# Kernel tuning notes

Measured on AMD Instinct MI355X. Metric: run time of the kernel, lower is better.

The kernel has to match this reference:

```python
import jax, jax.numpy as jnp
import numpy as np
from jax import lax

B = 8192
HS = 64        # hidden_size (output channels)
HS4 = HS + 4   # internal channel count (68)
K = 3          # conv kernel size


def setup_inputs() -> dict:
    key = jax.random.key(0)
    ks = jax.random.split(key, 16)
    def n(k, shape, s=1.0):
        return jax.random.normal(k, shape, dtype=jnp.float32) * s
    return {
        "x": n(ks[0], (B, HS, 6, 6)),
        "cell": n(ks[1], (B, 2)),
        "interspace_coord": n(ks[2], (B, 2, 6, 6)),
        "conv1_w": n(ks[3], (HS4, HS4, K, K), 0.05),
        "conv1_b": n(ks[4], (HS4,), 0.05),
        "conv3_w": n(ks[5], (HS4, HS4, K, K), 0.05),
        "conv3_b": n(ks[6], (HS4,), 0.05),
        "lin5_w": n(ks[7], (9 * HS, HS4 * 25), 0.02),
        "lin5_b": n(ks[8], (9 * HS,), 0.02),
        "lin4_w": n(ks[9], (9 * HS, HS4 * 16), 0.02),
        "lin4_b": n(ks[10], (9 * HS,), 0.02),
        "lin3_w": n(ks[11], (9 * HS, HS4 * 9), 0.02),
        "lin3_b": n(ks[12], (9 * HS,), 0.02),
        "final_w": n(ks[13], (HS, 9 * HS), 0.02),
        "final_b": n(ks[14], (HS,), 0.02),
    }


def _conv(z, w, b):
    # torch Conv2d with padding=k//2, stride 1 == SAME conv, NCHW/OIHW
    y = lax.conv_general_dilated(z, w, (1, 1), 'SAME',
                                 dimension_numbers=('NCHW', 'OIHW', 'NCHW'))
    return y + b[None, :, None, None]


def _corners(z, ws):
    # four corner windows, stacked on a new leading axis (corner-major)
    H, W = z.shape[-2:]
    return jnp.stack([z[..., :ws, :ws],
                      z[..., :ws, W - ws:],
                      z[..., H - ws:, :ws],
                      z[..., H - ws:, W - ws:]], axis=0)


def reference(x, cell, interspace_coord,
              conv1_w, conv1_b, conv3_w, conv3_b,
              lin5_w, lin5_b, lin4_w, lin4_b, lin3_w, lin3_b,
              final_w, final_b):
    Bn = x.shape[0]
    new_cell = jnp.broadcast_to(cell.reshape(Bn, -1)[:, :, None, None],
                                (Bn, 2, 6, 6))
    lins = {5: (lin5_w, lin5_b), 4: (lin4_w, lin4_b), 3: (lin3_w, lin3_b)}
    for ws in (5, 4, 3):
        z = jnp.concatenate([x, new_cell, interspace_coord], axis=1)  # [B,68,6,6]
        z = _corners(z, ws).reshape(-1, HS4, ws, ws)                  # [4B,68,ws,ws]
        z = jnp.sin(z) + jnp.cos(z)
        z = jax.nn.relu(_conv(z, conv1_w, conv1_b))
        z = jnp.sin(z) + jnp.cos(z)
        z = jax.nn.relu(_conv(z, conv3_w, conv3_b)).reshape(4, Bn, -1)
        Wl, bl = lins[ws]
        z = jax.nn.relu(z @ Wl.T + bl).reshape(4, Bn, HS, 3, 3)
        m = jnp.concatenate([z[0], z[1]], axis=-1)   # [B,64,3,6]
        n = jnp.concatenate([z[2], z[3]], axis=-1)
        x = jnp.concatenate([m, n], axis=-2)          # [B,64,6,6]
    ew = 3
    c = _corners(x, ew)                               # [4,B,64,3,3]
    c = c.reshape(4 * Bn, -1) @ final_w.T + final_b   # [4B,64]
    c = c.reshape(Bn, HS, 2, 2)                       # same flat-order reshape as torch
    xc = x[:, :, ew - 1:ew + 1, ew - 1:ew + 1]        # center 2x2
    return (xc * c).reshape(Bn, HS, -1)
```

## Files before the change

kernel.cpp:

```cpp
#include <hip/hip_runtime.h>
#include <hip/hip_bf16.h>
#include <cstdint>
#include <cstddef>

#define BN 8192
#define MTOT 32768

using bf16 = __hip_bfloat16;
typedef float f32x4 __attribute__((ext_vector_type(4)));
typedef short short8 __attribute__((ext_vector_type(8)));

__device__ __forceinline__ bf16 f2b(float v) { return __float2bfloat16(v); }
__device__ __forceinline__ float b2f(bf16 v) { return __bfloat162float(v); }
__device__ __forceinline__ float sincos_sum(float x) {
    return 1.41421356237f * __sinf(x + 0.78539816340f);
}

template<int WS> struct WsCfg;
template<> struct WsCfg<5> { static constexpr int KD = 1728, NP = 1792, KTRUE = 1700; };
template<> struct WsCfg<4> { static constexpr int KD = 1088, NP = 1152, KTRUE = 1088; };
template<> struct WsCfg<3> { static constexpr int KD = 640,  NP = 640,  KTRUE = 612;  };

template<int WS, bool SRC_F32>
__global__ __launch_bounds__(256)
void zprep_block(const float* __restrict__ xF, const bf16* __restrict__ xB,
                 const float* __restrict__ cell, const float* __restrict__ isc,
                 bf16* __restrict__ Z, int m0g, int CM)
{
    constexpr int KD = WsCfg<WS>::KD;
    constexpr int KTRUE = 68 * WS * WS;
    const int b = blockIdx.x, tid = threadIdx.x;
    __shared__ float s[68][37];

    for (int i = tid; i < 64 * 36; i += 256) {
        int ic = i / 36, off = i % 36;
        size_t idx = ((size_t)b * 64 + ic) * 36 + off;
        float t = SRC_F32 ? xF[idx] : b2f(xB[idx]);
        s[ic][off] = sincos_sum(t);
    }
    if (tid < 2) {
        float t = sincos_sum(cell[b * 2 + tid]);
        #pragma unroll
        for (int off = 0; off < 36; off++) s[64 + tid][off] = t;
    }
    if (tid >= 64 && tid < 136) {
        int j = tid - 64;
        int ic = j / 36, off = j % 36;
        s[66 + ic][off] = sincos_sum(isc[((size_t)b * 2 + ic) * 36 + off]);
    }
    __syncthreads();

    for (int i = tid; i < 4 * KD; i += 256) {
        int q = i / KD, k = i % KD;
        int gm = q * BN + b;
        if (gm < m0g || gm >= m0g + CM) continue;
        float v = 0.f;
        if (k < KTRUE) {
            int pi = k / 68, ic = k % 68;
            int r = (q >> 1) * (6 - WS) + pi / WS;
            int c = (q & 1) * (6 - WS) + pi % WS;
            v = s[ic][r * 6 + c];
        }
        Z[(size_t)(gm - m0g) * KD + k] = f2b(v);
    }
}

template<int WS>
__global__ void build_wdense(const float* __restrict__ w1, const float* __restrict__ w3,
                             bf16* __restrict__ W1d, bf16* __restrict__ W3d)
{
    constexpr int KD = WsCfg<WS>::KD, NP = WsCfg<WS>::NP;
    constexpr int KTRUE = 68 * WS * WS;
    constexpr unsigned per = (unsigned)NP * (unsigned)KD;
    unsigned e = blockIdx.x * 256u + threadIdx.x;
    if (e >= 2u * per) return;
    const float* src = (e < per) ? w1 : w3;
    bf16* dst = (e < per) ? W1d : W3d;
    unsigned i = (e < per) ? e : (e - per);
    int n = (int)(i / (unsigned)KD), k = (int)(i % (unsigned)KD);
    float v = 0.f;
    if (n < KTRUE && k < KTRUE) {
        int po = n / 68, oc = n % 68, ro = po / WS, co = po % WS;
        int pi = k / 68, ic = k % 68, ri = pi / WS, ci = pi % WS;
        int kr = ri - ro + 1, kc = ci - co + 1;
        if (kr >= 0 && kr < 3 && kc >= 0 && kc < 3)
            v = src[((oc * 68 + ic) * 3 + kr) * 3 + kc];
    }
    dst[i] = f2b(v);
}

template<int WS>
__global__ void repack_lin(const float* __restrict__ wl, bf16* __restrict__ WlP)
{
    constexpr int KD = WsCfg<WS>::KD;
    constexpr int KTRUE = 68 * WS * WS;
    unsigned e = blockIdx.x * 256u + threadIdx.x;
    if (e >= 640u * (unsigned)KD) return;
    int n = (int)(e / (unsigned)KD), k = (int)(e % (unsigned)KD);
    float v = 0.f;
    if (n < 576 && k < KTRUE) {
        int pi = k / 68, ic = k % 68;
        v = wl[(size_t)n * KTRUE + ic * (WS * WS) + pi];
    }
    WlP[e] = f2b(v);
}

__global__ void repack_fin(const float* __restrict__ fw, bf16* __restrict__ WfP)
{
    unsigned e = blockIdx.x * 256u + threadIdx.x;
    if (e >= 128u * 576u) return;
    unsigned n = e / 576u, k = e % 576u;
    WfP[e] = (n < 64u) ? f2b(fw[n * 576u + k]) : f2b(0.f);
}

__global__ void build_bias(const float* __restrict__ b1, const float* __restrict__ b3,
                           const float* __restrict__ bl5, const float* __restrict__ bl4,
                           const float* __restrict__ bl3, const float* __restrict__ bfin,
                           float* __restrict__ bias)
{
    int e = blockIdx.x * 256 + threadIdx.x;
    if (e >= 9216) return;
    float v = 0.f;
    if (e < 1792)      { int n = e;        if (n < 1700) v = b1[n % 68]; }
    else if (e < 3584) { int n = e - 1792; if (n < 1700) v = b3[n % 68]; }
    else if (e < 4736) { int n = e - 3584; if (n < 1088) v = b1[n % 68]; }
    else if (e < 5888) { int n = e - 4736; if (n < 1088) v = b3[n % 68]; }
    else if (e < 6528) { int n = e - 5888; if (n < 612)  v = b1[n % 68]; }
    else if (e < 7168) { int n = e - 6528; if (n < 612)  v = b3[n % 68]; }
    else if (e < 7808) { int n = e - 7168; if (n < 576)  v = bl5[n]; }
    else if (e < 8448) { int n = e - 7808; if (n < 576)  v = bl4[n]; }
    else if (e < 9088) { int n = e - 8448; if (n < 576)  v = bl3[n]; }
    else               { int n = e - 9088; if (n < 64)   v = bfin[n]; }
    bias[e] = v;
}

__global__ void afin_prep(const bf16* __restrict__ xb, bf16* __restrict__ Afin,
                          int m_start, int CM)
{
    unsigned e = blockIdx.x * 256u + threadIdx.x;
    if (e >= (unsigned)CM * 576u) return;
    int lm = (int)(e / 576u), k = (int)(e % 576u);
    int m = m_start + lm;
    int q = m >> 13, b = m & (BN - 1);
    int ch = k / 9, p = k % 9, pr = p / 3, pc = p % 3;
    int r = (q >> 1) * 3 + pr, c = (q & 1) * 3 + pc;
    Afin[e] = xb[((size_t)b * 64 + ch) * 36 + r * 6 + c];
}

__device__ __forceinline__ void gload_lds16(const bf16* g, const bf16* lds_wave_base)
{
    unsigned off = (unsigned)(uintptr_t)lds_wave_base;
    off = __builtin_amdgcn_readfirstlane(off);
    __builtin_amdgcn_global_load_lds((const __attribute__((address_space(1))) unsigned int*)g,
                                     (__attribute__((address_space(3))) unsigned int*)off,
                                     16, 0, 0);
}

__device__ __forceinline__ int imin(int a, int b) { return a < b ? a : b; }
__device__ __forceinline__ int imax(int a, int b) { return a > b ? a : b; }

template<int EPI, int WS>
__global__ __launch_bounds__(256)
void gemm_bt(const bf16* __restrict__ A, const bf16* __restrict__ Bm, int KD,
             const float* __restrict__ bias, int ntiles,
             bf16* __restrict__ C, int ldc, int nlimit,
             int m0g, bf16* __restrict__ xbuf_out,
             const bf16* __restrict__ xbuf_xc, float* __restrict__ outp)
{
    __shared__ bf16 As[128 * 32];
    __shared__ bf16 Bs[128 * 32];
    const int tid = threadIdx.x;
    const int wave = tid >> 6, lane = tid & 63;
    const int l15 = lane & 15, lq = lane >> 4;
    const int wr = (wave >> 1) * 64, wc = (wave & 1) * 64;

    const int id = blockIdx.x;
    const int mt8 = (int)gridDim.x / (ntiles * 8);
    const int xcd = id & 7, local = id >> 3;
    const int m_idx = xcd * mt8 + local / ntiles;
    const int n_idx = local % ntiles;
    const int n0 = n_idx * 128, m0 = m_idx * 128;

    int klo = 0, khi = KD;
    if (WS > 0) {
        constexpr int ROWLEN = WS * 68;
        int po_lo = imin(n0 / 68, WS * WS - 1);
        int po_hi = imin((n0 + 127) / 68, WS * WS - 1);
        int r_lo = imax(po_lo / WS - 1, 0);
        int r_hi = imin(po_hi / WS + 1, WS - 1);
        klo = (r_lo * ROWLEN) & ~31;
        khi = imin(KD, ((r_hi + 1) * ROWLEN + 31) & ~31);
    }

    const bf16* Ab = A + (size_t)m0 * KD;
    const bf16* Bb = Bm + (size_t)n0 * KD;
    const int srow = tid >> 2, scol = (tid & 3) * 8;
    const bf16* aG0 = Ab + (size_t)srow * KD + scol;
    const bf16* aG1 = Ab + (size_t)(srow + 64) * KD + scol;
    const bf16* bG0 = Bb + (size_t)srow * KD + scol;
    const bf16* bG1 = Bb + (size_t)(srow + 64) * KD + scol;
    const bf16* lA0 = &As[wave * 512];
    const bf16* lA1 = &As[2048 + wave * 512];
    const bf16* lB0 = &Bs[wave * 512];
    const bf16* lB1 = &Bs[2048 + wave * 512];

    f32x4 acc[4][4];
    #pragma unroll
    for (int i = 0; i < 4; i++)
        #pragma unroll
        for (int j = 0; j < 4; j++) { f32x4 z = {0.f, 0.f, 0.f, 0.f}; acc[i][j] = z; }

    for (int k0 = klo; k0 < khi; k0 += 32) {
        gload_lds16(aG0 + k0, lA0);
        gload_lds16(aG1 + k0, lA1);
        gload_lds16(bG0 + k0, lB0);
        gload_lds16(bG1 + k0, lB1);
        __syncthreads();
        short8 af[4], bg[4];
        #pragma unroll
        for (int i = 0; i < 4; i++) af[i] = *(const short8*)&As[(wr + i * 16 + l15) * 32 + lq * 8];
        #pragma unroll
        for (int j = 0; j < 4; j++) bg[j] = *(const short8*)&Bs[(wc + j * 16 + l15) * 32 + lq * 8];
        #pragma unroll
        for (int i = 0; i < 4; i++)
            #pragma unroll
            for (int j = 0; j < 4; j++)
                acc[i][j] = __builtin_amdgcn_mfma_f32_16x16x32_bf16(af[i], bg[j], acc[i][j], 0, 0, 0);
        __syncthreads();
    }

    #pragma unroll
    for (int i = 0; i < 4; i++) {
        #pragma unroll
        for (int j = 0; j < 4; j++) {
            int n = n0 + wc + j * 16 + l15;
            #pragma unroll
            for (int r = 0; r < 4; r++) {
                int m = m0 + wr + i * 16 + lq * 4 + r;
                float v = acc[i][j][r];
                if (EPI == 0) {
                    if (n < nlimit) {
                        v += bias[n]; v = fmaxf(v, 0.f); v = sincos_sum(v);
                        C[(size_t)m * ldc + n] = f2b(v);
                    }
                } else if (EPI == 1) {
                    if (n < nlimit) {
                        v += bias[n]; v = fmaxf(v, 0.f);
                        C[(size_t)m * ldc + n] = f2b(v);
                    }
                } else if (EPI == 2) {
                    if (n < 576) {
                        v += bias[n]; v = fmaxf(v, 0.f);
                        int gm = m0g + m;
                        int q = gm >> 13, b = gm & (BN - 1);
                        int ch = n / 9, p = n % 9, rr = p / 3, cc = p % 3;
                        int R = rr + (q >> 1) * 3, Cc = cc + (q & 1) * 3;
                        xbuf_out[((size_t)b * 64 + ch) * 36 + R * 6 + Cc] = f2b(v);
                    }
                } else {
                    if (n < 64) {
                        v += bias[n];
                        int gm = m0g + m;
                        int f = gm * 64 + n;
                        int b2 = f >> 8, rem = f & 255;
                        int ch2 = rem >> 2, ii = (rem >> 1) & 1, jj = rem & 1;
                        float xc = b2f(xbuf_xc[((size_t)b2 * 64 + ch2) * 36 + (2 + ii) * 6 + (2 + jj)]);
                        outp[f] = v * xc;
                    }
                }
            }
        }
    }
}

template<int WS, bool SRC_F32>
static void run_ws(const float* xsrcF, const bf16* xsrcB, bf16* xdst,
                   const float* cell, const float* isc,
                   bf16* Za, bf16* Zb, const bf16* W1d, const bf16* W3d, const bf16* WlP,
                   const float* bias, int bo1, int bo3, int bol,
                   int nchunk, hipStream_t stream)
{
    constexpr int KD = WsCfg<WS>::KD, NP = WsCfg<WS>::NP;
    int CM = MTOT / nchunk;
    int mt = CM / 128;
    for (int c = 0; c < nchunk; c++) {
        int m0g = c * CM;
        zprep_block<WS, SRC_F32><<<BN, 256, 0, stream>>>(
            xsrcF, xsrcB, cell, isc, Za, m0g, CM);
        int nt12 = NP / 128;
        gemm_bt<0, WS><<<nt12 * mt, 256, 0, stream>>>(Za, W1d, KD, bias + bo1, nt12,
                                                      Zb, KD, KD, 0, nullptr, nullptr, nullptr);
        gemm_bt<1, WS><<<nt12 * mt, 256, 0, stream>>>(Zb, W3d, KD, bias + bo3, nt12,
                                                      Za, KD, KD, 0, nullptr, nullptr, nullptr);
        gemm_bt<2, 0><<<5 * mt, 256, 0, stream>>>(Za, WlP, KD, bias + bol, 5,
                                                  nullptr, 0, 0, m0g, xdst, nullptr, nullptr);
    }
}

extern "C" void kernel_launch(void* const* d_in, const int* in_sizes, int n_in,
                              void* d_out, int out_size, void* d_ws, size_t ws_size,
                              hipStream_t stream)
{
    const float* x    = (const float*)d_in[0];
    const float* cell = (const float*)d_in[1];
    const float* isc  = (const float*)d_in[2];
    const float* c1w  = (const float*)d_in[3];
    const float* c1b  = (const float*)d_in[4];
    const float* c3w  = (const float*)d_in[5];
    const float* c3b  = (const float*)d_in[6];
    const float* l5w  = (const float*)d_in[7];
    const float* l5b  = (const float*)d_in[8];
    const float* l4w  = (const float*)d_in[9];
    const float* l4b  = (const float*)d_in[10];
    const float* l3w  = (const float*)d_in[11];
    const float* l3b  = (const float*)d_in[12];
    const float* fw   = (const float*)d_in[13];
    const float* fb   = (const float*)d_in[14];

    char* base = (char*)d_ws;
    size_t cur = 0;
    auto take = [&](size_t bytes) -> char* {
        char* r = base + cur; cur += (bytes + 255) & ~(size_t)255; return r;
    };

    const size_t XB = (size_t)BN * 64 * 36 * 2;
    size_t wbytes = 2 * (1792ull * 1728 + 1152ull * 1088 + 640ull * 640) * 2
                  + (640ull * 1728 + 640ull * 1088 + 640ull * 640) * 2
                  + 128ull * 576 * 2 + 9216ull * 4 + 64 * 256;
    auto need = [&](int nc) -> size_t {
        size_t xb = (nc > 1) ? 2 * XB : XB;
        return xb + wbytes + 2 * ((size_t)(MTOT / nc) * 1728 * 2);
    };
    int nchunk = (ws_size >= need(1)) ? 1 : (ws_size >= need(2)) ? 2
               : (ws_size >= need(4)) ? 4 : 8;

    bf16* xbufA = (bf16*)take(XB);
    bf16* xbufB = (nchunk > 1) ? (bf16*)take(XB) : xbufA;
    bf16* w1d5 = (bf16*)take(1792ull * 1728 * 2);
    bf16* w3d5 = (bf16*)take(1792ull * 1728 * 2);
    bf16* w1d4 = (bf16*)take(1152ull * 1088 * 2);
    bf16* w3d4 = (bf16*)take(1152ull * 1088 * 2);
    bf16* w1d3 = (bf16*)take(640ull * 640 * 2);
    bf16* w3d3 = (bf16*)take(640ull * 640 * 2);
    bf16* wl5p = (bf16*)take(640ull * 1728 * 2);
    bf16* wl4p = (bf16*)take(640ull * 1088 * 2);
    bf16* wl3p = (bf16*)take(640ull * 640 * 2);
    bf16* wfp  = (bf16*)take(128ull * 576 * 2);
    float* biasb = (float*)take(9216ull * 4);
    int CM = MTOT / nchunk;
    bf16* Za = (bf16*)take((size_t)CM * 1728 * 2);
    bf16* Zb = (bf16*)take((size_t)CM * 1728 * 2);
    bf16* Afin = Za;

    auto nb = [](size_t t) { return dim3((unsigned)((t + 255) / 256)); };
    build_wdense<5><<<nb(2ull * 1792 * 1728), 256, 0, stream>>>(c1w, c3w, w1d5, w3d5);
    build_wdense<4><<<nb(2ull * 1152 * 1088), 256, 0, stream>>>(c1w, c3w, w1d4, w3d4);
    build_wdense<3><<<nb(2ull * 640 * 640), 256, 0, stream>>>(c1w, c3w, w1d3, w3d3);
    repack_lin<5><<<nb(640ull * 1728), 256, 0, stream>>>(l5w, wl5p);
    repack_lin<4><<<nb(640ull * 1088), 256, 0, stream>>>(l4w, wl4p);
    repack_lin<3><<<nb(640ull * 640), 256, 0, stream>>>(l3w, wl3p);
    repack_fin<<<nb(128ull * 576), 256, 0, stream>>>(fw, wfp);
    build_bias<<<36, 256, 0, stream>>>(c1b, c3b, l5b, l4b, l3b, fb, biasb);

    run_ws<5, true >(x, nullptr, xbufA, cell, isc, Za, Zb, w1d5, w3d5, wl5p, biasb, 0,    1792, 7168, nchunk, stream);
    run_ws<4, false>(nullptr, xbufA, xbufB, cell, isc, Za, Zb, w1d4, w3d4, wl4p, biasb, 3584, 4736, 7808, nchunk, stream);
    run_ws<3, false>(nullptr, xbufB, xbufA, cell, isc, Za, Zb, w1d3, w3d3, wl3p, biasb, 5888, 6528, 8448, nchunk, stream);

    for (int c = 0; c < nchunk; c++) {
        int m0g = c * CM;
        afin_prep<<<nb((size_t)CM * 576), 256, 0, stream>>>(xbufA, Afin, m0g, CM);
        gemm_bt<3, 0><<<dim3(CM / 128), 256, 0, stream>>>(Afin, wfp, 576, biasb + 9088, 1,
                                                          nullptr, 0, 0, m0g, nullptr,
                                                          xbufA, (float*)d_out);
    }
}
```

Measured before the change: 1.358 ms.

## Load GEMM fragments directly from global memory into registers with prefetch

The GEMM kernel stops staging A and B tiles through LDS with global_load_lds and two barriers per k-step. Each lane now loads its MFMA fragments straight from global memory into registers, double-buffered so the next k-slice is fetched while the current MFMAs run. Bias values are also hoisted into registers before the main loop. Dropping LDS removes the barriers, but each wave now fetches its own copy of shared rows, which raises global and L2 traffic and register pressure.

Measured after the change: 2.439 ms. +79.5%, slower.

```diff
diff --git a/kernel.cpp b/kernel.cpp
--- a/kernel.cpp
+++ b/kernel.cpp
@@ -147,15 +147,6 @@
     Afin[e] = xb[((size_t)b * 64 + ch) * 36 + r * 6 + c];
 }
 
-__device__ __forceinline__ void gload_lds16(const bf16* g, const bf16* lds_wave_base)
-{
-    unsigned off = (unsigned)(uintptr_t)lds_wave_base;
-    off = __builtin_amdgcn_readfirstlane(off);
-    __builtin_amdgcn_global_load_lds((const __attribute__((address_space(1))) unsigned int*)g,
-                                     (__attribute__((address_space(3))) unsigned int*)off,
-                                     16, 0, 0);
-}
-
 __device__ __forceinline__ int imin(int a, int b) { return a < b ? a : b; }
 __device__ __forceinline__ int imax(int a, int b) { return a > b ? a : b; }
 
@@ -167,8 +158,6 @@
              int m0g, bf16* __restrict__ xbuf_out,
              const bf16* __restrict__ xbuf_xc, float* __restrict__ outp)
 {
-    __shared__ bf16 As[128 * 32];
-    __shared__ bf16 Bs[128 * 32];
     const int tid = threadIdx.x;
     const int wave = tid >> 6, lane = tid & 63;
     const int l15 = lane & 15, lq = lane >> 4;
@@ -192,17 +181,18 @@
         khi = imin(KD, ((r_hi + 1) * ROWLEN + 31) & ~31);
     }
 
-    const bf16* Ab = A + (size_t)m0 * KD;
-    const bf16* Bb = Bm + (size_t)n0 * KD;
-    const int srow = tid >> 2, scol = (tid & 3) * 8;
-    const bf16* aG0 = Ab + (size_t)srow * KD + scol;
-    const bf16* aG1 = Ab + (size_t)(srow + 64) * KD + scol;
-    const bf16* bG0 = Bb + (size_t)srow * KD + scol;
-    const bf16* bG1 = Bb + (size_t)(srow + 64) * KD + scol;
-    const bf16* lA0 = &As[wave * 512];
-    const bf16* lA1 = &As[2048 + wave * 512];
-    const bf16* lB0 = &Bs[wave * 512];
-    const bf16* lB1 = &Bs[2048 + wave * 512];
+    float bj[4];
+    #pragma unroll
+    for (int j = 0; j < 4; j++) bj[j] = bias[n0 + wc + j * 16 + l15];
+
+    const bf16* aP[4];
+    const bf16* bP[4];
+    #pragma unroll
+    for (int i = 0; i < 4; i++)
+        aP[i] = A + (size_t)(m0 + wr + i * 16 + l15) * KD + lq * 8;
+    #pragma unroll
+    for (int j = 0; j < 4; j++)
+        bP[j] = Bm + (size_t)(n0 + wc + j * 16 + l15) * KD + lq * 8;
 
     f32x4 acc[4][4];
     #pragma unroll
@@ -210,23 +200,27 @@
         #pragma unroll
         for (int j = 0; j < 4; j++) { f32x4 z = {0.f, 0.f, 0.f, 0.f}; acc[i][j] = z; }
 
+    short8 curA[4], curB[4], nxtA[4], nxtB[4];
+    #pragma unroll
+    for (int i = 0; i < 4; i++) curA[i] = *(const short8*)(aP[i] + klo);
+    #pragma unroll
+    for (int j = 0; j < 4; j++) curB[j] = *(const short8*)(bP[j] + klo);
+
     for (int k0 = klo; k0 < khi; k0 += 32) {
-        gload_lds16(aG0 + k0, lA0);
-        gload_lds16(aG1 + k0, lA1);
-        gload_lds16(bG0 + k0, lB0);
-        gload_lds16(bG1 + k0, lB1);
-        __syncthreads();
-        short8 af[4], bg[4];
-        #pragma unroll
-        for (int i = 0; i < 4; i++) af[i] = *(const short8*)&As[(wr + i * 16 + l15) * 32 + lq * 8];
-        #pragma unroll
-        for (int j = 0; j < 4; j++) bg[j] = *(const short8*)&Bs[(wc + j * 16 + l15) * 32 + lq * 8];
+        int kn = (k0 + 32 < khi) ? (k0 + 32) : k0;
+        #pragma unroll
+        for (int i = 0; i < 4; i++) nxtA[i] = *(const short8*)(aP[i] + kn);
+        #pragma unroll
+        for (int j = 0; j < 4; j++) nxtB[j] = *(const short8*)(bP[j] + kn);
         #pragma unroll
         for (int i = 0; i < 4; i++)
             #pragma unroll
             for (int j = 0; j < 4; j++)
-                acc[i][j] = __builtin_amdgcn_mfma_f32_16x16x32_bf16(af[i], bg[j], acc[i][j], 0, 0, 0);
-        __syncthreads();
+                acc[i][j] = __builtin_amdgcn_mfma_f32_16x16x32_bf16(curA[i], curB[j], acc[i][j], 0, 0, 0);
+        #pragma unroll
+        for (int i = 0; i < 4; i++) curA[i] = nxtA[i];
+        #pragma unroll
+        for (int j = 0; j < 4; j++) curB[j] = nxtB[j];
     }
 
     #pragma unroll
@@ -240,17 +234,17 @@
                 float v = acc[i][j][r];
                 if (EPI == 0) {
                     if (n < nlimit) {
-                        v += bias[n]; v = fmaxf(v, 0.f); v = sincos_sum(v);
+                        v += bj[j]; v = fmaxf(v, 0.f); v = sincos_sum(v);
                         C[(size_t)m * ldc + n] = f2b(v);
                     }
                 } else if (EPI == 1) {
                     if (n < nlimit) {
-                        v += bias[n]; v = fmaxf(v, 0.f);
+                        v += bj[j]; v = fmaxf(v, 0.f);
                         C[(size_t)m * ldc + n] = f2b(v);
                     }
                 } else if (EPI == 2) {
                     if (n < 576) {
-                        v += bias[n]; v = fmaxf(v, 0.f);
+                        v += bj[j]; v = fmaxf(v, 0.f);
                         int gm = m0g + m;
                         int q = gm >> 13, b = gm & (BN - 1);
                         int ch = n / 9, p = n % 9, rr = p / 3, cc = p % 3;
@@ -259,7 +253,7 @@
                     }
                 } else {
                     if (n < 64) {
-                        v += bias[n];
+                        v += bj[j];
                         int gm = m0g + m;
                         int f = gm * 64 + n;
                         int b2 = f >> 8, rem = f & 255;
@@ -362,15 +356,19 @@
     repack_fin<<<nb(128ull * 576), 256, 0, stream>>>(fw, wfp);
     build_bias<<<36, 256, 0, stream>>>(c1b, c3b, l5b, l4b, l3b, fb, biasb);
 
-    run_ws<5, true >(x, nullptr, xbufA, cell, isc, Za, Zb, w1d5, w3d5, wl5p, biasb, 0,    1792, 7168, nchunk, stream);
-    run_ws<4, false>(nullptr, xbufA, xbufB, cell, isc, Za, Zb, w1d4, w3d4, wl4p, biasb, 3584, 4736, 7808, nchunk, stream);
-    run_ws<3, false>(nullptr, xbufB, xbufA, cell, isc, Za, Zb, w1d3, w3d3, wl3p, biasb, 5888, 6528, 8448, nchunk, stream);
+    run_ws<5, true >(x, nullptr, xbufA, cell, isc, Za, Zb, w1d5, w3d5, wl5p, biasb,
+                     0, 1792, 7168, nchunk, stream);
+    run_ws<4, false>(nullptr, xbufA, xbufB, cell, isc, Za, Zb, w1d4, w3d4, wl4p, biasb,
+                     3584, 4736, 7808, nchunk, stream);
+    run_ws<3, false>(nullptr, xbufB, xbufA, cell, isc, Za, Zb, w1d3, w3d3, wl3p, biasb,
+                     5888, 6528, 8448, nchunk, stream);
 
     for (int c = 0; c < nchunk; c++) {
         int m0g = c * CM;
+        int mt = CM / 128;
         afin_prep<<<nb((size_t)CM * 576), 256, 0, stream>>>(xbufA, Afin, m0g, CM);
-        gemm_bt<3, 0><<<dim3(CM / 128), 256, 0, stream>>>(Afin, wfp, 576, biasb + 9088, 1,
-                                                          nullptr, 0, 0, m0g, nullptr,
-                                                          xbufA, (float*)d_out);
-    }
-}
+        gemm_bt<3, 0><<<mt, 256, 0, stream>>>(Afin, wfp, 576, biasb + 9088, 1,
+                                              nullptr, 0, 0, m0g, nullptr,
+                                              xbufA, (float*)d_out);
+    }
+}
```

## Skip zero K-spans in conv GEMMs and write final-layer input directly

Applied to the files above, without the earlier changes.

The banded conv GEMMs now compute per-row K spans when an N tile covers a single output row, so they skip the zero weight columns that sit outside the 3-column neighbourhood. The last window size's linear layer writes its ReLU output straight into a corner-major buffer that the final GEMM consumes directly, which removes the afin_prep gather kernel and reads the center values from that buffer. Bias loads are hoisted into registers per column. In exchange the workspace must hold an extra M×576 buffer, and the multi-span loop adds some control overhead.

Result: no change. 1.340 ms (-1.4%).

```diff
diff --git a/kernel.cpp b/kernel.cpp
--- a/kernel.cpp
+++ b/kernel.cpp
@@ -134,19 +134,6 @@
     bias[e] = v;
 }
 
-__global__ void afin_prep(const bf16* __restrict__ xb, bf16* __restrict__ Afin,
-                          int m_start, int CM)
-{
-    unsigned e = blockIdx.x * 256u + threadIdx.x;
-    if (e >= (unsigned)CM * 576u) return;
-    int lm = (int)(e / 576u), k = (int)(e % 576u);
-    int m = m_start + lm;
-    int q = m >> 13, b = m & (BN - 1);
-    int ch = k / 9, p = k % 9, pr = p / 3, pc = p % 3;
-    int r = (q >> 1) * 3 + pr, c = (q & 1) * 3 + pc;
-    Afin[e] = xb[((size_t)b * 64 + ch) * 36 + r * 6 + c];
-}
-
 __device__ __forceinline__ void gload_lds16(const bf16* g, const bf16* lds_wave_base)
 {
     unsigned off = (unsigned)(uintptr_t)lds_wave_base;
@@ -165,7 +152,7 @@
              const float* __restrict__ bias, int ntiles,
              bf16* __restrict__ C, int ldc, int nlimit,
              int m0g, bf16* __restrict__ xbuf_out,
-             const bf16* __restrict__ xbuf_xc, float* __restrict__ outp)
+             const bf16* __restrict__ afin_xc, float* __restrict__ outp)
 {
     __shared__ bf16 As[128 * 32];
     __shared__ bf16 Bs[128 * 32];
@@ -181,16 +168,34 @@
     const int n_idx = local % ntiles;
     const int n0 = n_idx * 128, m0 = m_idx * 128;
 
-    int klo = 0, khi = KD;
+    int nspans = 1, sbeg[4], send[4];
+    sbeg[0] = 0; send[0] = KD;
     if (WS > 0) {
-        constexpr int ROWLEN = WS * 68;
         int po_lo = imin(n0 / 68, WS * WS - 1);
         int po_hi = imin((n0 + 127) / 68, WS * WS - 1);
-        int r_lo = imax(po_lo / WS - 1, 0);
-        int r_hi = imin(po_hi / WS + 1, WS - 1);
-        klo = (r_lo * ROWLEN) & ~31;
-        khi = imin(KD, ((r_hi + 1) * ROWLEN + 31) & ~31);
-    }
+        int ro_lo = po_lo / WS, ro_hi = po_hi / WS;
+        int r_lo = imax(ro_lo - 1, 0), r_hi = imin(ro_hi + 1, WS - 1);
+        int ci_lo = 0, ci_hi = WS - 1;
+        if (ro_lo == ro_hi) {
+            ci_lo = imax(po_lo % WS - 1, 0);
+            ci_hi = imin(po_hi % WS + 1, WS - 1);
+        }
+        if (ci_lo == 0 && ci_hi == WS - 1) {
+            sbeg[0] = (r_lo * WS * 68) & ~31;
+            send[0] = imin(KD, ((r_hi + 1) * WS * 68 + 31) & ~31);
+        } else {
+            nspans = 0;
+            for (int ri = r_lo; ri <= r_hi; ri++) {
+                sbeg[nspans] = ((ri * WS + ci_lo) * 68) & ~31;
+                send[nspans] = imin(KD, (((ri * WS + ci_hi + 1) * 68) + 31) & ~31);
+                nspans++;
+            }
+        }
+    }
+
+    float bj[4];
+    #pragma unroll
+    for (int j = 0; j < 4; j++) bj[j] = bias[n0 + wc + j * 16 + l15];
 
     const bf16* Ab = A + (size_t)m0 * KD;
     const bf16* Bb = Bm + (size_t)n0 * KD;
@@ -210,23 +215,25 @@
         #pragma unroll
         for (int j = 0; j < 4; j++) { f32x4 z = {0.f, 0.f, 0.f, 0.f}; acc[i][j] = z; }
 
-    for (int k0 = klo; k0 < khi; k0 += 32) {
-        gload_lds16(aG0 + k0, lA0);
-        gload_lds16(aG1 + k0, lA1);
-        gload_lds16(bG0 + k0, lB0);
-        gload_lds16(bG1 + k0, lB1);
-        __syncthreads();
-        short8 af[4], bg[4];
-        #pragma unroll
-        for (int i = 0; i < 4; i++) af[i] = *(const short8*)&As[(wr + i * 16 + l15) * 32 + lq * 8];
-        #pragma unroll
-        for (int j = 0; j < 4; j++) bg[j] = *(const short8*)&Bs[(wc + j * 16 + l15) * 32 + lq * 8];
-        #pragma unroll
-        for (int i = 0; i < 4; i++)
+    for (int s = 0; s < nspans; s++) {
+        for (int k0 = sbeg[s]; k0 < send[s]; k0 += 32) {
+            gload_lds16(aG0 + k0, lA0);
+            gload_lds16(aG1 + k0, lA1);
+            gload_lds16(bG0 + k0, lB0);
+            gload_lds16(bG1 + k0, lB1);
+            __syncthreads();
+            short8 af[4], bg[4];
             #pragma unroll
-            for (int j = 0; j < 4; j++)
-                acc[i][j] = __builtin_amdgcn_mfma_f32_16x16x32_bf16(af[i], bg[j], acc[i][j], 0, 0, 0);
-        __syncthreads();
+            for (int i = 0; i < 4; i++) af[i] = *(const short8*)&As[(wr + i * 16 + l15) * 32 + lq * 8];
+            #pragma unroll
+            for (int j = 0; j < 4; j++) bg[j] = *(const short8*)&Bs[(wc + j * 16 + l15) * 32 + lq * 8];
+            #pragma unroll
+            for (int i = 0; i < 4; i++)
+                #pragma unroll
+                for (int j = 0; j < 4; j++)
+                    acc[i][j] = __builtin_amdgcn_mfma_f32_16x16x32_bf16(af[i], bg[j], acc[i][j], 0, 0, 0);
+            __syncthreads();
+        }
     }
 
     #pragma unroll
@@ -240,17 +247,17 @@
                 float v = acc[i][j][r];
                 if (EPI == 0) {
                     if (n < nlimit) {
-                        v += bias[n]; v = fmaxf(v, 0.f); v = sincos_sum(v);
+                        v += bj[j]; v = fmaxf(v, 0.f); v = sincos_sum(v);
                         C[(size_t)m * ldc + n] = f2b(v);
                     }
                 } else if (EPI == 1) {
                     if (n < nlimit) {
-                        v += bias[n]; v = fmaxf(v, 0.f);
+                        v += bj[j]; v = fmaxf(v, 0.f);
                         C[(size_t)m * ldc + n] = f2b(v);
                     }
                 } else if (EPI == 2) {
                     if (n < 576) {
-                        v += bias[n]; v = fmaxf(v, 0.f);
+                        v += bj[j]; v = fmaxf(v, 0.f);
                         int gm = m0g + m;
                         int q = gm >> 13, b = gm & (BN - 1);
                         int ch = n / 9, p = n % 9, rr = p / 3, cc = p % 3;
@@ -259,12 +266,14 @@
                     }
                 } else {
                     if (n < 64) {
-                        v += bias[n];
+                        v += bj[j];
                         int gm = m0g + m;
                         int f = gm * 64 + n;
                         int b2 = f >> 8, rem = f & 255;
                         int ch2 = rem >> 2, ii = (rem >> 1) & 1, jj = rem & 1;
-                        float xc = b2f(xbuf_xc[((size_t)b2 * 64 + ch2) * 36 + (2 + ii) * 6 + (2 + jj)]);
+                        int qq = ii * 2 + jj;
+                        const int offt[4] = {8, 6, 2, 0};
+                        float xc = b2f(afin_xc[((size_t)qq * BN + b2) * 576 + ch2 * 9 + offt[qq]]);
                         outp[f] = v * xc;
                     }
                 }
@@ -274,7 +283,7 @@
 }
 
 template<int WS, bool SRC_F32>
-static void run_ws(const float* xsrcF, const bf16* xsrcB, bf16* xdst,
+static void run_ws(const float* xsrcF, const bf16* xsrcB, bf16* xdst, bf16* afin,
                    const float* cell, const float* isc,
                    bf16* Za, bf16* Zb, const bf16* W1d, const bf16* W3d, const bf16* WlP,
                    const float* bias, int bo1, int bo3, int bol,
@@ -292,8 +301,14 @@
                                                       Zb, KD, KD, 0, nullptr, nullptr, nullptr);
         gemm_bt<1, WS><<<nt12 * mt, 256, 0, stream>>>(Zb, W3d, KD, bias + bo3, nt12,
                                                       Za, KD, KD, 0, nullptr, nullptr, nullptr);
-        gemm_bt<2, 0><<<5 * mt, 256, 0, stream>>>(Za, WlP, KD, bias + bol, 5,
-                                                  nullptr, 0, 0, m0g, xdst, nullptr, nullptr);
+        if (afin) {
+            gemm_bt<1, 0><<<5 * mt, 256, 0, stream>>>(Za, WlP, KD, bias + bol, 5,
+                                                      afin + (size_t)m0g * 576, 576, 576,
+                                                      0, nullptr, nullptr, nullptr);
+        } else {
+            gemm_bt<2, 0><<<5 * mt, 256, 0, stream>>>(Za, WlP, KD, bias + bol, 5,
+                                                      nullptr, 0, 0, m0g, xdst, nullptr, nullptr);
+        }
     }
 }
 
@@ -324,18 +339,20 @@
     };
 
     const size_t XB = (size_t)BN * 64 * 36 * 2;
+    const size_t AFB = (size_t)MTOT * 576 * 2;
     size_t wbytes = 2 * (1792ull * 1728 + 1152ull * 1088 + 640ull * 640) * 2
                   + (640ull * 1728 + 640ull * 1088 + 640ull * 640) * 2
                   + 128ull * 576 * 2 + 9216ull * 4 + 64 * 256;
     auto need = [&](int nc) -> size_t {
         size_t xb = (nc > 1) ? 2 * XB : XB;
-        return xb + wbytes + 2 * ((size_t)(MTOT / nc) * 1728 * 2);
+        return xb + AFB + wbytes + 2 * ((size_t)(MTOT / nc) * 1728 * 2);
     };
     int nchunk = (ws_size >= need(1)) ? 1 : (ws_size >= need(2)) ? 2
                : (ws_size >= need(4)) ? 4 : 8;
 
     bf16* xbufA = (bf16*)take(XB);
     bf16* xbufB = (nchunk > 1) ? (bf16*)take(XB) : xbufA;
+    bf16* afinb = (bf16*)take(AFB);
     bf16* w1d5 = (bf16*)take(1792ull * 1728 * 2);
     bf16* w3d5 = (bf16*)take(1792ull * 1728 * 2);
     bf16* w1d4 = (bf16*)take(1152ull * 1088 * 2);
@@ -350,7 +367,6 @@
     int CM = MTOT / nchunk;
     bf16* Za = (bf16*)take((size_t)CM * 1728 * 2);
     bf16* Zb = (bf16*)take((size_t)CM * 1728 * 2);
-    bf16* Afin = Za;
 
     auto nb = [](size_t t) { return dim3((unsigned)((t + 255) / 256)); };
     build_wdense<5><<<nb(2ull * 1792 * 1728), 256, 0, stream>>>(c1w, c3w, w1d5, w3d5);
@@ -362,15 +378,18 @@
     repack_fin<<<nb(128ull * 576), 256, 0, stream>>>(fw, wfp);
     build_bias<<<36, 256, 0, stream>>>(c1b, c3b, l5b, l4b, l3b, fb, biasb);
 
-    run_ws<5, true >(x, nullptr, xbufA, cell, isc, Za, Zb, w1d5, w3d5, wl5p, biasb, 0,    1792, 7168, nchunk, stream);
-    run_ws<4, false>(nullptr, xbufA, xbufB, cell, isc, Za, Zb, w1d4, w3d4, wl4p, biasb, 3584, 4736, 7808, nchunk, stream);
-    run_ws<3, false>(nullptr, xbufB, xbufA, cell, isc, Za, Zb, w1d3, w3d3, wl3p, biasb, 5888, 6528, 8448, nchunk, stream);
+    run_ws<5, true >(x, nullptr, xbufA, nullptr, cell, isc, Za, Zb, w1d5, w3d5, wl5p,
+                     biasb, 0, 1792, 7168, nchunk, stream);
+    run_ws<4, false>(nullptr, xbufA, xbufB, nullptr, cell, isc, Za, Zb, w1d4, w3d4, wl4p,
+                     biasb, 3584, 4736, 7808, nchunk, stream);
+    run_ws<3, false>(nullptr, xbufB, nullptr, afinb, cell, isc, Za, Zb, w1d3, w3d3, wl3p,
+                     biasb, 5888, 6528, 8448, nchunk, stream);
 
     for (int c = 0; c < nchunk; c++) {
         int m0g = c * CM;
-        afin_prep<<<nb((size_t)CM * 576), 256, 0, stream>>>(xbufA, Afin, m0g, CM);
-        gemm_bt<3, 0><<<dim3(CM / 128), 256, 0, stream>>>(Afin, wfp, 576, biasb + 9088, 1,
-                                                          nullptr, 0, 0, m0g, nullptr,
-                                                          xbufA, (float*)d_out);
-    }
-}
+        int mt = CM / 128;
+        gemm_bt<3, 0><<<mt, 256, 0, stream>>>(afinb + (size_t)m0g * 576, wfp, 576,
+                                              biasb + 9088, 1, nullptr, 0, 0, m0g,
+                                              nullptr, afinb, (float*)d_out);
+    }
+}
```
